# Performance work log

Measured on AMD Instinct MI355X. Metric: run time of the kernel, lower is better.

## Reference

```python
import jax, jax.numpy as jnp
import numpy as np

B, S, D, H, SPAN = 4, 1024, 768, 12, 512
HD = D // H  # 64


def setup_inputs() -> dict:
    key = jax.random.key(0)
    ks = jax.random.split(key, 8)
    hidden_states = jax.random.normal(ks[0], (B, S, D), jnp.float32)
    rel_embeddings = jax.random.normal(ks[1], (2 * SPAN, D), jnp.float32) * 0.02
    Wq = jax.random.normal(ks[2], (D, D), jnp.float32) * 0.02
    Wk = jax.random.normal(ks[3], (D, D), jnp.float32) * 0.02
    Wv = jax.random.normal(ks[4], (D, D), jnp.float32) * 0.02
    Wo = jax.random.normal(ks[5], (D, D), jnp.float32) * 0.02
    bq = jnp.zeros((D,), jnp.float32); bk = jnp.zeros((D,), jnp.float32)
    bv = jnp.zeros((D,), jnp.float32); bo = jnp.zeros((D,), jnp.float32)
    ln_g = jnp.ones((D,), jnp.float32); ln_b = jnp.zeros((D,), jnp.float32)
    idx = jnp.arange(S)
    relative_pos = (idx[:, None] - idx[None, :]).astype(jnp.int32)  # q - k
    lengths = jnp.array([1024, 896, 768, 512])  # padding-style mask
    valid = idx[None, :] < lengths[:, None]  # [B,S]
    attention_mask = (valid[:, :, None] & valid[:, None, :])[:, None, :, :].astype(jnp.int32)  # [B,1,S,S]
    return dict(hidden_states=hidden_states, rel_embeddings=rel_embeddings,
                Wq=Wq, bq=bq, Wk=Wk, bk=bk, Wv=Wv, bv=bv, Wo=Wo, bo=bo,
                ln_g=ln_g, ln_b=ln_b, attention_mask=attention_mask,
                relative_pos=relative_pos)


def reference(hidden_states, rel_embeddings, Wq, bq, Wk, bk, Wv, bv, Wo, bo,
              ln_g, ln_b, attention_mask, relative_pos):
    # content projections -> [B,H,S,HD]
    q = (hidden_states @ Wq.T + bq).reshape(B, S, H, HD).transpose(0, 2, 1, 3)
    k = (hidden_states @ Wk.T + bk).reshape(B, S, H, HD).transpose(0, 2, 1, 3)
    v = (hidden_states @ Wv.T + bv).reshape(B, S, H, HD).transpose(0, 2, 1, 3)

    scale_qk = jnp.sqrt(jnp.float32(HD * 3))  # scale_factor = 3
    scores = jnp.einsum('bhqd,bhkd->bhqk', q, k) / scale_qk

    # shared-key position projections -> [H, 2*SPAN, HD]
    pos_q = (rel_embeddings @ Wq.T + bq).reshape(2 * SPAN, H, HD).transpose(1, 0, 2)
    pos_k = (rel_embeddings @ Wk.T + bk).reshape(2 * SPAN, H, HD).transpose(1, 0, 2)

    rp = relative_pos.astype(jnp.int32)
    # c2p: query vs relative key-position embedding, gathered by clamp(rel+span)
    c2p_att = jnp.einsum('bhqd,hkd->bhqk', q, pos_k)  # [B,H,S,2*SPAN]
    c2p_pos = jnp.clip(rp + SPAN, 0, 2 * SPAN - 1)
    c2p_idx = jnp.broadcast_to(c2p_pos[None, None], (B, H, S, S))
    c2p = jnp.take_along_axis(c2p_att, c2p_idx, axis=-1) / scale_qk

    # p2c: key vs relative query-position embedding, gathered by clamp(-rel+span), then transposed
    p2c_att = jnp.einsum('bhkd,hqd->bhkq', k, pos_q)  # [B,H,S,2*SPAN]
    p2c_pos = jnp.clip(SPAN - rp, 0, 2 * SPAN - 1)
    p2c_idx = jnp.broadcast_to(p2c_pos[None, None], (B, H, S, S))
    p2c = jnp.swapaxes(jnp.take_along_axis(p2c_att, p2c_idx, axis=-1), -1, -2)
    p2c = p2c / jnp.sqrt(jnp.float32(HD))  # note: torch uses sqrt(d) here, no scale_factor

    scores = scores + c2p + p2c

    # XSoftmax: masked softmax with zeros at masked positions
    mask = attention_mask.astype(bool)  # [B,1,S,S]
    neg = jnp.finfo(scores.dtype).min
    probs = jax.nn.softmax(jnp.where(mask, scores, neg), axis=-1)
    probs = jnp.where(mask, probs, jnp.float32(0))

    ctx = jnp.einsum('bhqk,bhkd->bhqd', probs, v).transpose(0, 2, 1, 3).reshape(B, S, D)

    # DebertaV2SelfOutput: dense + residual + LayerNorm(eps=1e-7)
    x = ctx @ Wo.T + bo + hidden_states
    mu = x.mean(-1, keepdims=True)
    var = ((x - mu) ** 2).mean(-1, keepdims=True)
    return (x - mu) / jnp.sqrt(var + 1e-7) * ln_g + ln_b
```

## Files before the change

### kernel.cpp

```cpp
#include <hip/hip_runtime.h>
#include <hip/hip_bf16.h>
#include <stdint.h>

typedef __hip_bfloat16 bf16;
typedef __attribute__((ext_vector_type(8))) short s8v;
typedef __attribute__((ext_vector_type(4))) float f4v;

__device__ __align__(16) bf16 g_hidden[4096 * 768];
__device__ __align__(16) bf16 g_rel[1024 * 768];
__device__ __align__(16) bf16 g_Wqkv[2304 * 768];
__device__ __align__(16) bf16 g_Wo[768 * 768];
__device__ __align__(16) bf16 g_biasQKV[2304];
__device__ __align__(16) bf16 g_biasPos[1536];
__device__ __align__(16) bf16 g_bo[768];
__device__ __align__(16) bf16 g_lng[768];
__device__ __align__(16) bf16 g_lnb[768];
__device__ __align__(16) bf16 g_Y1[4096 * 1536];
__device__ __align__(16) bf16 g_VT[48u * 64 * 1024];
__device__ __align__(16) bf16 g_Yp[1024 * 1536];
__device__ __align__(16) bf16 g_ctx[4096 * 768];
__device__ __align__(16) float g_X[4096 * 768];
__device__ int g_vq[4096], g_vk[4096], g_kmax[4];

__device__ __forceinline__ float bfs(short x) {
  return __uint_as_float(((unsigned int)(unsigned short)x) << 16);
}
__device__ __forceinline__ unsigned short f2bf(float f) {
  bf16 h = __float2bfloat16(f);
  return *(unsigned short*)&h;
}
__device__ __forceinline__ bool detect_bf16(const void* lng_raw) {
  return *(const unsigned int*)lng_raw == 0x3F803F80u;
}

__device__ __forceinline__ void cvt4(const void* src, bf16* dst, long grp, bool isbf) {
  long e = grp * 4;
  if (isbf) {
    *(uint2*)(dst + e) = *(const uint2*)((const bf16*)src + e);
  } else {
    float4 f = *(const float4*)((const float*)src + e);
    union { unsigned short us[4]; uint2 v; } u;
    u.us[0] = f2bf(f.x); u.us[1] = f2bf(f.y); u.us[2] = f2bf(f.z); u.us[3] = f2bf(f.w);
    *(uint2*)(dst + e) = u.v;
  }
}

__global__ __launch_bounds__(256) void cvt_inputs(
    const void* h, const void* r,
    const void* wq, const void* wk, const void* wv, const void* wo,
    const void* bq, const void* bk, const void* bv, const void* bo,
    const void* lg, const void* lb)
{
  if (blockIdx.x == 0 && threadIdx.x < 4) g_kmax[threadIdx.x] = 0;
  const bool isbf = detect_bf16(lg);
  long i = (long)blockIdx.x * 256 + threadIdx.x;
  if (i < 786432) { cvt4(h,  g_hidden,          i, isbf); return; } i -= 786432;
  if (i < 196608) { cvt4(r,  g_rel,             i, isbf); return; } i -= 196608;
  if (i < 147456) { cvt4(wq, g_Wqkv,            i, isbf); return; } i -= 147456;
  if (i < 147456) { cvt4(wk, g_Wqkv + 589824,   i, isbf); return; } i -= 147456;
  if (i < 147456) { cvt4(wv, g_Wqkv + 1179648,  i, isbf); return; } i -= 147456;
  if (i < 147456) { cvt4(wo, g_Wo,              i, isbf); return; } i -= 147456;
  if (i < 192)    { cvt4(bq, g_biasQKV,         i, isbf); return; } i -= 192;
  if (i < 192)    { cvt4(bk, g_biasQKV + 768,   i, isbf); return; } i -= 192;
  if (i < 192)    { cvt4(bv, g_biasQKV + 1536,  i, isbf); return; } i -= 192;
  if (i < 192)    { cvt4(bq, g_biasPos,         i, isbf); return; } i -= 192;
  if (i < 192)    { cvt4(bk, g_biasPos + 768,   i, isbf); return; } i -= 192;
  if (i < 192)    { cvt4(lg, g_lng,             i, isbf); return; } i -= 192;
  if (i < 192)    { cvt4(lb, g_lnb,             i, isbf); return; }
}

__global__ __launch_bounds__(256) void mask_prep(const int* __restrict__ mask) {
  int t = blockIdx.x * 256 + threadIdx.x;
  int b = t >> 10, i = t & 1023;
  int vq = mask[((size_t)(b * 1024 + i)) * 1024];
  int vk = mask[((size_t)(b * 1024)) * 1024 + i];
  g_vq[t] = vq;
  g_vk[t] = vk;
  if (vq | vk) atomicMax(&g_kmax[b], i + 1);
}

__global__ __launch_bounds__(256, 2) void gemm_bt(int which) {
  __shared__ short As[128][72];
  __shared__ short Bs[128][72];

  const bf16 *A, *B; const bf16* bias;
  int lda, ldb, K, mode;
  const int m0 = blockIdx.y * 128, n0 = blockIdx.x * 128;

  if (which == 0) {
    A = g_hidden; lda = 768; B = g_Wqkv; ldb = 768; bias = g_biasQKV; K = 768;
    mode = (n0 >= 1536) ? 5 : 0;
  } else if (which == 1) {
    A = g_rel; lda = 768; B = g_Wqkv; ldb = 768; bias = g_biasPos; K = 768; mode = 1;
  } else {
    A = g_ctx; lda = 768; B = g_Wo; ldb = 768; bias = g_bo; K = 768; mode = 4;
  }

  const int tid = threadIdx.x, wave = tid >> 6, lane = tid & 63;
  const int quad = lane >> 4, l15 = lane & 15;
  const int wm = (wave >> 1) * 64, wn = (wave & 1) * 64;
  const int sr = tid >> 2, sc8 = (tid & 3) * 16;

  f4v acc[4][4];
#pragma unroll
  for (int i = 0; i < 4; i++)
#pragma unroll
    for (int j = 0; j < 4; j++) acc[i][j] = (f4v){0.f, 0.f, 0.f, 0.f};

  uint4 pa0, pa1, pa2, pa3, pb0, pb1, pb2, pb3;
#define LOAD_T(k0)                                                           \
  {                                                                          \
    const bf16* ap = A + (size_t)(m0 + sr) * lda + (k0) + sc8;               \
    const bf16* ap2 = A + (size_t)(m0 + sr + 64) * lda + (k0) + sc8;         \
    const bf16* bp = B + (size_t)(n0 + sr) * ldb + (k0) + sc8;               \
    const bf16* bp2 = B + (size_t)(n0 + sr + 64) * ldb + (k0) + sc8;         \
    pa0 = *(const uint4*)ap;  pa1 = *(const uint4*)(ap + 8);                 \
    pa2 = *(const uint4*)ap2; pa3 = *(const uint4*)(ap2 + 8);                \
    pb0 = *(const uint4*)bp;  pb1 = *(const uint4*)(bp + 8);                 \
    pb2 = *(const uint4*)bp2; pb3 = *(const uint4*)(bp2 + 8);                \
  }

  LOAD_T(0)
  for (int k0 = 0; k0 < K; k0 += 64) {
    __syncthreads();
    *(uint4*)&As[sr][sc8] = pa0;      *(uint4*)&As[sr][sc8 + 8] = pa1;
    *(uint4*)&As[sr + 64][sc8] = pa2; *(uint4*)&As[sr + 64][sc8 + 8] = pa3;
    *(uint4*)&Bs[sr][sc8] = pb0;      *(uint4*)&Bs[sr][sc8 + 8] = pb1;
    *(uint4*)&Bs[sr + 64][sc8] = pb2; *(uint4*)&Bs[sr + 64][sc8 + 8] = pb3;
    if (k0 + 64 < K) LOAD_T(k0 + 64)
    __syncthreads();

    s8v af[4][2], bfr[4][2];
#pragma unroll
    for (int mt = 0; mt < 4; mt++) {
      af[mt][0] = *(const s8v*)&As[wm + mt * 16 + l15][quad * 8];
      af[mt][1] = *(const s8v*)&As[wm + mt * 16 + l15][32 + quad * 8];
    }
#pragma unroll
    for (int nt = 0; nt < 4; nt++) {
      bfr[nt][0] = *(const s8v*)&Bs[wn + nt * 16 + l15][quad * 8];
      bfr[nt][1] = *(const s8v*)&Bs[wn + nt * 16 + l15][32 + quad * 8];
    }
#pragma unroll
    for (int mt = 0; mt < 4; mt++)
#pragma unroll
      for (int nt = 0; nt < 4; nt++) {
        acc[mt][nt] = __builtin_amdgcn_mfma_f32_16x16x32_bf16(af[mt][0], bfr[nt][0], acc[mt][nt], 0, 0, 0);
        acc[mt][nt] = __builtin_amdgcn_mfma_f32_16x16x32_bf16(af[mt][1], bfr[nt][1], acc[mt][nt], 0, 0, 0);
      }
  }
#undef LOAD_T

  float biasv[4];
#pragma unroll
  for (int nt = 0; nt < 4; nt++)
    biasv[nt] = bfs(*(const short*)&bias[n0 + wn + nt * 16 + l15]);

#pragma unroll
  for (int mt = 0; mt < 4; mt++) {
#pragma unroll
    for (int nt = 0; nt < 4; nt++) {
      const int mbase = m0 + wm + mt * 16 + quad * 4;
      const int n = n0 + wn + nt * 16 + l15;
      if (mode == 5) {
        const int dd = n - 1536, hv = dd >> 6, hd = dd & 63;
        const int bb = mbase >> 10, ss = mbase & 1023;
        float t0 = acc[mt][nt][0] + biasv[nt], t1 = acc[mt][nt][1] + biasv[nt];
        float t2 = acc[mt][nt][2] + biasv[nt], t3 = acc[mt][nt][3] + biasv[nt];
        uint2 pk;
        pk.x = (unsigned int)f2bf(t0) | ((unsigned int)f2bf(t1) << 16);
        pk.y = (unsigned int)f2bf(t2) | ((unsigned int)f2bf(t3) << 16);
        *(uint2*)(g_VT + (((size_t)(bb * 12 + hv) * 64 + hd) << 10) + ss) = pk;
        continue;
      }
#pragma unroll
      for (int reg = 0; reg < 4; reg++) {
        const int m = mbase + reg;
        float v = acc[mt][nt][reg] + biasv[nt];
        if (mode == 0) {
          g_Y1[(size_t)m * 1536 + n] = __float2bfloat16(v);
        } else if (mode == 1) {
          g_Yp[(size_t)m * 1536 + n] = __float2bfloat16(v);
        } else {
          v += bfs(*(const short*)&g_hidden[(size_t)m * 768 + n]);
          g_X[(size_t)m * 768 + n] = v;
        }
      }
    }
  }
}

__global__ __launch_bounds__(256, 2) void attn_mfma() {
  const int bh = blockIdx.y, b = bh / 12, hh = bh - b * 12;
  const int q0 = blockIdx.x * 64;
  const int tid = threadIdx.x, wave = tid >> 6, lane = tid & 63;
  const int quad = lane >> 4, l15 = lane & 15;
  const int kmax = g_kmax[b];

  if (q0 >= kmax) {
    uint4 zz = {0u, 0u, 0u, 0u};
#pragma unroll
    for (int s = tid; s < 512; s += 256) {
      int r = s >> 3, cc = (s & 7) * 8;
      *(uint4*)(g_ctx + (size_t)(b * 1024 + q0 + r) * 768 + hh * 64 + cc) = zz;
    }
    return;
  }

  __shared__ short C2Pr[64 * 90];
  __shared__ short P2Cr[64 * 90];
  __shared__ short Pl[4][16][72];

  const size_t qrow = (size_t)(b * 1024 + q0 + wave * 16 + l15) * 1536 + hh * 64;
  const s8v qf0 = *(const s8v*)(g_Y1 + qrow + quad * 8);
  const s8v qf1 = *(const s8v*)(g_Y1 + qrow + 32 + quad * 8);

  int vqr[4];
#pragma unroll
  for (int reg = 0; reg < 4; reg++)
    vqr[reg] = g_vq[b * 1024 + q0 + wave * 16 + quad * 4 + reg];

  f4v accO[4];
#pragma unroll
  for (int dt = 0; dt < 4; dt++) accO[dt] = (f4v){0.f, 0.f, 0.f, 0.f};
  float psum[4] = {0.f, 0.f, 0.f, 0.f};

  const bf16* Kbase = g_Y1 + (size_t)(b * 1024) * 1536 + 768 + hh * 64;
  const bf16* Vbase = g_VT + ((size_t)bh << 16);
  const bf16* PKbase = g_Yp + 768 + hh * 64;
  const bf16* PQbase = g_Yp + hh * 64;

  const float r192 = 0.0721687836487032f;
  const float r64 = 0.125f;

  for (int k0 = 0; k0 < kmax; k0 += 64) {
    f4v sacc[4];
#pragma unroll
    for (int nt = 0; nt < 4; nt++) {
      const bf16* kbrow = Kbase + (size_t)(k0 + nt * 16 + l15) * 1536;
      s8v kb0 = *(const s8v*)(kbrow + quad * 8);
      s8v kb1 = *(const s8v*)(kbrow + 32 + quad * 8);
      sacc[nt] = __builtin_amdgcn_mfma_f32_16x16x32_bf16(qf0, kb0, (f4v){0.f, 0.f, 0.f, 0.f}, 0, 0, 0);
      sacc[nt] = __builtin_amdgcn_mfma_f32_16x16x32_bf16(qf1, kb1, sacc[nt], 0, 0, 0);
    }
    const bf16* karow = Kbase + (size_t)(k0 + wave * 16 + l15) * 1536;
    const s8v ka0 = *(const s8v*)(karow + quad * 8);
    const s8v ka1 = *(const s8v*)(karow + 32 + quad * 8);

    __syncthreads();

    const int cbase = q0 - k0 + 449, pbase = k0 - q0 + 449;
#pragma unroll
    for (int t2 = 0; t2 < 5; t2++) {
      const int nr = (wave + t2) * 16 + l15;
      int jk = min(max(cbase + nr, 0), 1023);
      const bf16* pkrow = PKbase + (size_t)jk * 1536;
      s8v b0 = *(const s8v*)(pkrow + quad * 8);
      s8v b1 = *(const s8v*)(pkrow + 32 + quad * 8);
      f4v cacc = __builtin_amdgcn_mfma_f32_16x16x32_bf16(qf0, b0, (f4v){0.f, 0.f, 0.f, 0.f}, 0, 0, 0);
      cacc = __builtin_amdgcn_mfma_f32_16x16x32_bf16(qf1, b1, cacc, 0, 0, 0);
      int jq = min(max(pbase + nr, 0), 1023);
      const bf16* pqrow = PQbase + (size_t)jq * 1536;
      s8v c0 = *(const s8v*)(pqrow + quad * 8);
      s8v c1 = *(const s8v*)(pqrow + 32 + quad * 8);
      f4v pacc = __builtin_amdgcn_mfma_f32_16x16x32_bf16(ka0, c0, (f4v){0.f, 0.f, 0.f, 0.f}, 0, 0, 0);
      pacc = __builtin_amdgcn_mfma_f32_16x16x32_bf16(ka1, c1, pacc, 0, 0, 0);
      const int col = t2 * 16 + l15;
#pragma unroll
      for (int reg = 0; reg < 4; reg++) {
        const int row = wave * 16 + quad * 4 + reg;
        C2Pr[row * 90 + col] = (short)f2bf(cacc[reg]);
        P2Cr[row * 90 + col] = (short)f2bf(pacc[reg]);
      }
    }
    __syncthreads();

    const bool tail = (k0 + 64 > kmax);
#pragma unroll
    for (int nt = 0; nt < 4; nt++) {
      const int kl = nt * 16 + l15;
#pragma unroll
      for (int reg = 0; reg < 4; reg++) {
        const int qr = quad * 4 + reg;
        float c2 = bfs(C2Pr[(wave * 16 + qr) * 90 + qr - kl + 63]);
        float p2 = bfs(P2Cr[kl * 90 + l15 - wave * 16 - qr + 63]);
        float sc = (sacc[nt][reg] + c2) * r192 + p2 * r64;
        float pe = __expf(fminf(sc, 60.f));
        if (tail && (k0 + kl >= kmax)) pe = 0.f;
        psum[reg] += pe;
        Pl[wave][qr][kl] = (short)f2bf(pe);
      }
    }

    s8v pa0 = *(const s8v*)&Pl[wave][l15][quad * 8];
    s8v pa1 = *(const s8v*)&Pl[wave][l15][32 + quad * 8];
#pragma unroll
    for (int dt = 0; dt < 4; dt++) {
      const bf16* vrow = Vbase + ((size_t)(dt * 16 + l15) << 10) + k0;
      s8v vb0 = *(const s8v*)(vrow + quad * 8);
      s8v vb1 = *(const s8v*)(vrow + 32 + quad * 8);
      accO[dt] = __builtin_amdgcn_mfma_f32_16x16x32_bf16(pa0, vb0, accO[dt], 0, 0, 0);
      accO[dt] = __builtin_amdgcn_mfma_f32_16x16x32_bf16(pa1, vb1, accO[dt], 0, 0, 0);
    }
  }

#pragma unroll
  for (int off = 1; off < 16; off <<= 1)
#pragma unroll
    for (int reg = 0; reg < 4; reg++) psum[reg] += __shfl_xor(psum[reg], off);

  float inv[4];
#pragma unroll
  for (int reg = 0; reg < 4; reg++)
    inv[reg] = (vqr[reg] != 0 && psum[reg] > 0.f) ? 1.f / psum[reg] : 0.f;

#pragma unroll
  for (int dt = 0; dt < 4; dt++)
#pragma unroll
    for (int reg = 0; reg < 4; reg++) {
      float v = accO[dt][reg] * inv[reg];
      g_ctx[(size_t)(b * 1024 + q0 + wave * 16 + quad * 4 + reg) * 768 + hh * 64 + dt * 16 + l15] =
          __float2bfloat16(v);
    }
}

__global__ __launch_bounds__(256) void ln_kernel(const void* lng_raw, void* out) {
  const bool isbf = detect_bf16(lng_raw);
  const int row = blockIdx.x;
  const int tid = threadIdx.x;
  const float* xr = g_X + (size_t)row * 768;
  float x0 = xr[tid], x1 = xr[tid + 256], x2 = xr[tid + 512];
  float s = x0 + x1 + x2;
  float s2 = x0 * x0 + x1 * x1 + x2 * x2;
#pragma unroll
  for (int off = 32; off; off >>= 1) { s += __shfl_xor(s, off); s2 += __shfl_xor(s2, off); }
  __shared__ float red[2][4];
  int w = tid >> 6, ln = tid & 63;
  if (ln == 0) { red[0][w] = s; red[1][w] = s2; }
  __syncthreads();
  float ts = red[0][0] + red[0][1] + red[0][2] + red[0][3];
  float ts2 = red[1][0] + red[1][1] + red[1][2] + red[1][3];
  float mu = ts * (1.f / 768.f);
  float var = fmaxf(ts2 * (1.f / 768.f) - mu * mu, 0.f);
  float rstd = rsqrtf(var + 1e-7f);
#pragma unroll
  for (int q = 0; q < 3; q++) {
    int cidx = tid + q * 256;
    float xv = (q == 0) ? x0 : (q == 1 ? x1 : x2);
    float gg = bfs(*(const short*)&g_lng[cidx]);
    float bb = bfs(*(const short*)&g_lnb[cidx]);
    float val = (xv - mu) * rstd * gg + bb;
    if (isbf) ((bf16*)out)[(size_t)row * 768 + cidx] = __float2bfloat16(val);
    else      ((float*)out)[(size_t)row * 768 + cidx] = val;
  }
}

extern "C" void kernel_launch(void* const* d_in, const int* in_sizes, int n_in,
                              void* d_out, int out_size, void* d_ws, size_t ws_size,
                              hipStream_t stream) {
  const int* amask = (const int*)d_in[12];
  (void)d_ws; (void)ws_size; (void)in_sizes; (void)n_in; (void)out_size;

  cvt_inputs<<<dim3(6150), 256, 0, stream>>>(
      d_in[0], d_in[1], d_in[2], d_in[4], d_in[6], d_in[8],
      d_in[3], d_in[5], d_in[7], d_in[9], d_in[10], d_in[11]);
  mask_prep<<<dim3(16), 256, 0, stream>>>(amask);
  gemm_bt<<<dim3(18, 32, 1), 256, 0, stream>>>(0);
  gemm_bt<<<dim3(12, 8, 1), 256, 0, stream>>>(1);
  attn_mfma<<<dim3(16, 48), 256, 0, stream>>>();
  gemm_bt<<<dim3(6, 32, 1), 256, 0, stream>>>(4);
  ln_kernel<<<dim3(4096), 256, 0, stream>>>(d_in[10], d_out);
}
```

Baseline: 417.6 us.

## Split attention over key chunks with combine pass; stage V-transpose via LDS

The attention kernel is split along the key dimension into up to four 256-key chunks. Each chunk writes unnormalised partial outputs and row sums to global scratch, and a new combine kernel adds them and normalises. This raises the grid from 768 to up to 3072 blocks to improve occupancy and load balance across query tiles with uneven key lengths. The cost is extra fp32 traffic through global memory and one more launch. This appears valid without max-rescaling because the original softmax also accumulated exp without a running max. Separately, the V-transpose epilogue of the QKV GEMM now stages the tile through LDS to make coalesced 16-byte stores, and the GEMM is templated on its mode.

```diff
diff --git a/kernel.cpp b/kernel.cpp
--- a/kernel.cpp
+++ b/kernel.cpp
@@ -20,6 +20,8 @@
 __device__ __align__(16) bf16 g_Yp[1024 * 1536];
 __device__ __align__(16) bf16 g_ctx[4096 * 768];
 __device__ __align__(16) float g_X[4096 * 768];
+__device__ __align__(16) float g_opart[48u * 16 * 4 * 4096];
+__device__ __align__(16) float g_spart[48u * 16 * 4 * 64];
 __device__ int g_vq[4096], g_vk[4096], g_kmax[4];
 
 __device__ __forceinline__ float bfs(short x) {
@@ -79,21 +81,22 @@
   if (vq | vk) atomicMax(&g_kmax[b], i + 1);
 }
 
-__global__ __launch_bounds__(256, 2) void gemm_bt(int which) {
-  __shared__ short As[128][72];
-  __shared__ short Bs[128][72];
+template <int WHICH>
+__global__ __launch_bounds__(256, 2) void gemm_bt() {
+  __shared__ short Sh[2][128][72];
+  short (*As)[72] = Sh[0];
+  short (*Bs)[72] = Sh[1];
 
   const bf16 *A, *B; const bf16* bias;
-  int lda, ldb, K, mode;
+  int lda, ldb, K;
   const int m0 = blockIdx.y * 128, n0 = blockIdx.x * 128;
 
-  if (which == 0) {
+  if (WHICH == 0) {
     A = g_hidden; lda = 768; B = g_Wqkv; ldb = 768; bias = g_biasQKV; K = 768;
-    mode = (n0 >= 1536) ? 5 : 0;
-  } else if (which == 1) {
-    A = g_rel; lda = 768; B = g_Wqkv; ldb = 768; bias = g_biasPos; K = 768; mode = 1;
+  } else if (WHICH == 1) {
+    A = g_rel; lda = 768; B = g_Wqkv; ldb = 768; bias = g_biasPos; K = 768;
   } else {
-    A = g_ctx; lda = 768; B = g_Wo; ldb = 768; bias = g_bo; K = 768; mode = 4;
+    A = g_ctx; lda = 768; B = g_Wo; ldb = 768; bias = g_bo; K = 768;
   }
 
   const int tid = threadIdx.x, wave = tid >> 6, lane = tid & 63;
@@ -156,30 +159,45 @@
   for (int nt = 0; nt < 4; nt++)
     biasv[nt] = bfs(*(const short*)&bias[n0 + wn + nt * 16 + l15]);
 
+  if (WHICH == 0 && n0 >= 1536) {
+    short* T = &Sh[0][0][0];
+    __syncthreads();
+#pragma unroll
+    for (int nt = 0; nt < 4; nt++) {
+      const int rn = wn + nt * 16 + l15;
+#pragma unroll
+      for (int mt = 0; mt < 4; mt++) {
+        const int cm = wm + mt * 16 + quad * 4;
+#pragma unroll
+        for (int reg = 0; reg < 4; reg++)
+          T[rn * 136 + cm + reg] = (short)f2bf(acc[mt][nt][reg] + biasv[nt]);
+      }
+    }
+    __syncthreads();
+    const int bb = m0 >> 10, m0s = m0 & 1023, hv0 = (n0 - 1536) >> 6;
+#pragma unroll
+    for (int i = 0; i < 8; i++) {
+      int cid = tid + i * 256;
+      int row = cid >> 4, ch = (cid & 15) * 8;
+      uint4 val = *(uint4*)&T[row * 136 + ch];
+      *(uint4*)(g_VT + ((((size_t)(bb * 12 + hv0 + (row >> 6))) * 64 + (row & 63)) << 10) + m0s + ch) = val;
+    }
+    return;
+  }
+
 #pragma unroll
   for (int mt = 0; mt < 4; mt++) {
 #pragma unroll
     for (int nt = 0; nt < 4; nt++) {
       const int mbase = m0 + wm + mt * 16 + quad * 4;
       const int n = n0 + wn + nt * 16 + l15;
-      if (mode == 5) {
-        const int dd = n - 1536, hv = dd >> 6, hd = dd & 63;
-        const int bb = mbase >> 10, ss = mbase & 1023;
-        float t0 = acc[mt][nt][0] + biasv[nt], t1 = acc[mt][nt][1] + biasv[nt];
-        float t2 = acc[mt][nt][2] + biasv[nt], t3 = acc[mt][nt][3] + biasv[nt];
-        uint2 pk;
-        pk.x = (unsigned int)f2bf(t0) | ((unsigned int)f2bf(t1) << 16);
-        pk.y = (unsigned int)f2bf(t2) | ((unsigned int)f2bf(t3) << 16);
-        *(uint2*)(g_VT + (((size_t)(bb * 12 + hv) * 64 + hd) << 10) + ss) = pk;
-        continue;
-      }
 #pragma unroll
       for (int reg = 0; reg < 4; reg++) {
         const int m = mbase + reg;
         float v = acc[mt][nt][reg] + biasv[nt];
-        if (mode == 0) {
+        if (WHICH == 0) {
           g_Y1[(size_t)m * 1536 + n] = __float2bfloat16(v);
-        } else if (mode == 1) {
+        } else if (WHICH == 1) {
           g_Yp[(size_t)m * 1536 + n] = __float2bfloat16(v);
         } else {
           v += bfs(*(const short*)&g_hidden[(size_t)m * 768 + n]);
@@ -190,22 +208,17 @@
   }
 }
 
-__global__ __launch_bounds__(256, 2) void attn_mfma() {
+__global__ __launch_bounds__(256, 2) void attn_part() {
   const int bh = blockIdx.y, b = bh / 12, hh = bh - b * 12;
   const int q0 = blockIdx.x * 64;
+  const int ks = blockIdx.z;
+  const int kmax = g_kmax[b];
+  const int ks0 = ks * 256;
+  if (q0 >= kmax || ks0 >= kmax) return;
+  const int kend = min(ks0 + 256, kmax);
+
   const int tid = threadIdx.x, wave = tid >> 6, lane = tid & 63;
   const int quad = lane >> 4, l15 = lane & 15;
-  const int kmax = g_kmax[b];
-
-  if (q0 >= kmax) {
-    uint4 zz = {0u, 0u, 0u, 0u};
-#pragma unroll
-    for (int s = tid; s < 512; s += 256) {
-      int r = s >> 3, cc = (s & 7) * 8;
-      *(uint4*)(g_ctx + (size_t)(b * 1024 + q0 + r) * 768 + hh * 64 + cc) = zz;
-    }
-    return;
-  }
 
   __shared__ short C2Pr[64 * 90];
   __shared__ short P2Cr[64 * 90];
@@ -214,11 +227,6 @@
   const size_t qrow = (size_t)(b * 1024 + q0 + wave * 16 + l15) * 1536 + hh * 64;
   const s8v qf0 = *(const s8v*)(g_Y1 + qrow + quad * 8);
   const s8v qf1 = *(const s8v*)(g_Y1 + qrow + 32 + quad * 8);
-
-  int vqr[4];
-#pragma unroll
-  for (int reg = 0; reg < 4; reg++)
-    vqr[reg] = g_vq[b * 1024 + q0 + wave * 16 + quad * 4 + reg];
 
   f4v accO[4];
 #pragma unroll
@@ -233,7 +241,7 @@
   const float r192 = 0.0721687836487032f;
   const float r64 = 0.125f;
 
-  for (int k0 = 0; k0 < kmax; k0 += 64) {
+  for (int k0 = ks0; k0 < kend; k0 += 64) {
     f4v sacc[4];
 #pragma unroll
     for (int nt = 0; nt < 4; nt++) {
@@ -309,19 +317,60 @@
 #pragma unroll
     for (int reg = 0; reg < 4; reg++) psum[reg] += __shfl_xor(psum[reg], off);
 
-  float inv[4];
-#pragma unroll
-  for (int reg = 0; reg < 4; reg++)
-    inv[reg] = (vqr[reg] != 0 && psum[reg] > 0.f) ? 1.f / psum[reg] : 0.f;
-
+  const int part = (bh * 16 + blockIdx.x) * 4 + ks;
+  if (l15 == 0) {
+#pragma unroll
+    for (int reg = 0; reg < 4; reg++)
+      g_spart[part * 64 + wave * 16 + quad * 4 + reg] = psum[reg];
+  }
+  float* op = g_opart + (size_t)part * 4096;
 #pragma unroll
   for (int dt = 0; dt < 4; dt++)
 #pragma unroll
-    for (int reg = 0; reg < 4; reg++) {
-      float v = accO[dt][reg] * inv[reg];
-      g_ctx[(size_t)(b * 1024 + q0 + wave * 16 + quad * 4 + reg) * 768 + hh * 64 + dt * 16 + l15] =
-          __float2bfloat16(v);
-    }
+    for (int reg = 0; reg < 4; reg++)
+      op[(wave * 16 + quad * 4 + reg) * 64 + dt * 16 + l15] = accO[dt][reg];
+}
+
+__global__ __launch_bounds__(256) void attn_combine() {
+  const int qt = blockIdx.x, bh = blockIdx.y, b = bh / 12, hh = bh - b * 12;
+  const int q0 = qt * 64;
+  const int kmax = g_kmax[b];
+  const int tid = threadIdx.x;
+  const int q = tid >> 2, d0 = (tid & 3) * 16;
+  const size_t crow = (size_t)(b * 1024 + q0 + q) * 768 + hh * 64 + d0;
+
+  if (q0 >= kmax) {
+    uint4 zz = {0u, 0u, 0u, 0u};
+    *(uint4*)(g_ctx + crow) = zz;
+    *(uint4*)(g_ctx + crow + 8) = zz;
+    return;
+  }
+  const int nspl = min(4, (kmax + 255) >> 8);
+  const int part0 = (bh * 16 + qt) * 4;
+
+  float sum[16];
+#pragma unroll
+  for (int j = 0; j < 16; j++) sum[j] = 0.f;
+  float l = 0.f;
+  for (int p = 0; p < nspl; p++) {
+    l += g_spart[(part0 + p) * 64 + q];
+    const float* op = g_opart + (size_t)(part0 + p) * 4096 + q * 64 + d0;
+#pragma unroll
+    for (int j = 0; j < 16; j += 4) {
+      float4 v = *(const float4*)(op + j);
+      sum[j] += v.x; sum[j + 1] += v.y; sum[j + 2] += v.z; sum[j + 3] += v.w;
+    }
+  }
+  const int vq = g_vq[b * 1024 + q0 + q];
+  const float inv = (vq != 0 && l > 0.f) ? 1.f / l : 0.f;
+  union { unsigned short us[8]; uint4 v; } o0, o1;
+#pragma unroll
+  for (int j = 0; j < 8; j++) {
+    o0.us[j] = f2bf(sum[j] * inv);
+    o1.us[j] = f2bf(sum[8 + j] * inv);
+  }
+  *(uint4*)(g_ctx + crow) = o0.v;
+  *(uint4*)(g_ctx + crow + 8) = o1.v;
 }
 
 __global__ __launch_bounds__(256) void ln_kernel(const void* lng_raw, void* out) {
@@ -365,9 +414,10 @@
       d_in[0], d_in[1], d_in[2], d_in[4], d_in[6], d_in[8],
       d_in[3], d_in[5], d_in[7], d_in[9], d_in[10], d_in[11]);
   mask_prep<<<dim3(16), 256, 0, stream>>>(amask);
-  gemm_bt<<<dim3(18, 32, 1), 256, 0, stream>>>(0);
-  gemm_bt<<<dim3(12, 8, 1), 256, 0, stream>>>(1);
-  attn_mfma<<<dim3(16, 48), 256, 0, stream>>>();
-  gemm_bt<<<dim3(6, 32, 1), 256, 0, stream>>>(4);
+  gemm_bt<0><<<dim3(18, 32), 256, 0, stream>>>();
+  gemm_bt<1><<<dim3(12, 8), 256, 0, stream>>>();
+  attn_part<<<dim3(16, 48, 4), 256, 0, stream>>>();
+  attn_combine<<<dim3(16, 48), 256, 0, stream>>>();
+  gemm_bt<4><<<dim3(6, 32), 256, 0, stream>>>();
   ln_kernel<<<dim3(4096), 256, 0, stream>>>(d_in[10], d_out);
 }
```

After: 398.7 us. -4.5%, faster.
